# Performance work log

Hardware: AMD Instinct MI355X
Metric: run time of the kernel (lower is better)

## Reference

```python
import jax, jax.numpy as jnp
import numpy as np

N = 10000   # nodes
E = 160000  # edges per layer (avg degree 16)
B = 8       # batch of time windows
CIN = 32
S = 32      # spatial_channels
COUT = 32
NEG_SLOPE = 0.01  # F.leaky_relu default


def _xavier(k, shape):
    bound = np.sqrt(6.0 / (shape[0] + shape[1])).astype(np.float32)
    return jax.random.uniform(k, shape, jnp.float32, -bound, bound)


def setup_inputs() -> dict:
    key = jax.random.key(0)
    ks = jax.random.split(key, 20)
    return {
        "X": jax.random.normal(ks[0], (B, N, CIN), jnp.float32),
        "edge_index0": jax.random.randint(ks[1], (2, E), 0, N, jnp.int32),
        "edge_index1": jax.random.randint(ks[2], (2, E), 0, N, jnp.int32),
        "edge_weight0": jax.random.uniform(ks[3], (E,), jnp.float32),
        "edge_weight1": jax.random.uniform(ks[4], (E,), jnp.float32),
        "res_n_id0": jnp.arange(N, dtype=jnp.int32),
        "res_n_id1": jnp.arange(N, dtype=jnp.int32),
        # layer 1 params
        "Wn1": _xavier(ks[5], (CIN, S)),
        "We1": _xavier(ks[6], (1, S)),
        "Q1": _xavier(ks[7], (S, S)),
        "K1": _xavier(ks[8], (S, S)),
        "att_w1": _xavier(ks[9], (3 * S, 1)),
        "att_b1": jnp.zeros((1,), jnp.float32),
        "out_w1": _xavier(ks[10], (2 * S, S)),
        "out_b1": jnp.zeros((S,), jnp.float32),
        # layer 2 params
        "Wn2": _xavier(ks[11], (S, COUT)),
        "We2": _xavier(ks[12], (1, COUT)),
        "Q2": _xavier(ks[13], (COUT, COUT)),
        "K2": _xavier(ks[14], (COUT, COUT)),
        "att_w2": _xavier(ks[15], (3 * COUT, 1)),
        "att_b2": jnp.zeros((1,), jnp.float32),
        "out_w2": _xavier(ks[16], (2 * COUT, COUT)),
        "out_b2": jnp.zeros((COUT,), jnp.float32),
    }


def _egnn_conv(x_src, x_dst, edge_index, edge_w, Wn, We, Q, K, att_w, att_b, out_w, out_b):
    # x_src: [Ns, B, Cin], x_dst: [Nd, B, Cin], edge_index: [2, E], edge_w: [E]
    xs = x_src @ Wn                              # [Ns, B, O]
    xd = x_dst @ Wn                              # [Nd, B, O]
    ee = edge_w[:, None] @ We                    # [E, O]  (edge_channels = 1)
    src, dst = edge_index[0], edge_index[1]
    xj = xs[src]                                 # [E, B, O] gather source feats
    xi = xd[dst]                                 # [E, B, O] gather target feats
    q = xj @ Q                                   # [E, B, O]
    k = xi @ K                                   # [E, B, O]
    eb = jnp.broadcast_to(ee[:, None, :], q.shape)  # [E, B, O]
    att_feature = jnp.concatenate([q, k, eb], axis=-1)          # [E, B, 3O]
    att = jax.nn.sigmoid(att_feature @ att_w + att_b)           # [E, B, 1]
    msg = att * xj * jax.nn.sigmoid(eb)                         # [E, B, O]
    aggr = jnp.zeros_like(xd).at[dst].add(msg)                  # scatter-add -> [Nd, B, O]
    upd = jnp.concatenate([xd, aggr], axis=-1) @ out_w + out_b  # [Nd, B, O]
    return xd + upd


def reference(X, edge_index0, edge_index1, edge_weight0, edge_weight1,
              res_n_id0, res_n_id1,
              Wn1, We1, Q1, K1, att_w1, att_b1, out_w1, out_b1,
              Wn2, We2, Q2, K2, att_w2, att_b2, out_w2, out_b2):
    h = jnp.transpose(X, (1, 0, 2))              # [N, B, CIN]
    h = _egnn_conv(h, h[res_n_id0], edge_index0, edge_weight0,
                   Wn1, We1, Q1, K1, att_w1, att_b1, out_w1, out_b1)
    h = jax.nn.leaky_relu(h, NEG_SLOPE)
    h = _egnn_conv(h, h[res_n_id1], edge_index1, edge_weight1,
                   Wn2, We2, Q2, K2, att_w2, att_b2, out_w2, out_b2)
    h = jax.nn.leaky_relu(h, NEG_SLOPE)
    return jnp.transpose(h, (1, 0, 2))           # [B, N, COUT]
```

## Files before the change

kernel.cpp:

```cpp
#include <hip/hip_runtime.h>

#define NNODES 10000
#define NEDGES 160000
#define NB 8
#define NC 32
#define CAP 96
#define LUTB 2048
#define EBLKS 625
#define LUTBLKS 128
constexpr float NEG_SLOPE = 0.01f;

__device__ __forceinline__ float sigmoidf_(float x) {
    return 1.0f / (1.0f + __expf(-x));
}

__device__ __forceinline__ unsigned pk2bf(float a, float b) {
    unsigned ua = __float_as_uint(a);
    ua = (ua + 0x7fffu + ((ua >> 16) & 1u)) >> 16;
    unsigned ub = __float_as_uint(b);
    ub = (ub + 0x7fffu + ((ub >> 16) & 1u)) & 0xffff0000u;
    return ua | ub;
}

__global__ __launch_bounds__(256) void prologue_kernel(
    const float* Q1, const float* K1, const float* aw1, const float* We1,
    const float* Q2, const float* K2, const float* aw2, const float* We2,
    const int* __restrict__ ei0, const int* __restrict__ ei1,
    const float* __restrict__ ew0, const float* __restrict__ ew1,
    float* consts, uint2* __restrict__ lut,
    int2* __restrict__ pkw1, int2* __restrict__ pkw2,
    int* __restrict__ cnt,
    unsigned* __restrict__ xs1h, unsigned* __restrict__ xs2h,
    float* __restrict__ sq1, float* __restrict__ sk1,
    const float* __restrict__ X, const float* __restrict__ Wn)
{
    int bx = blockIdx.x;
    int t = threadIdx.x;

    if (bx < 2 * EBLKS) {
        int layer = bx / EBLKS;
        int e = (bx % EBLKS) * 256 + t;
        if (e < NEDGES) {
            const int*   ei = layer ? ei1 : ei0;
            const float* ew = layer ? ew1 : ew0;
            int src = ei[e];
            int dst = ei[NEDGES + e];
            float w = ew[e];
            int pos = atomicAdd(&cnt[layer * NNODES + dst], 1);
            if (pos < CAP) {
                int ix = (int)(w * (float)LUTB);
                ix = min(max(ix, 0), LUTB - 1);
                (layer ? pkw2 : pkw1)[(size_t)dst * CAP + pos] =
                    make_int2(src | (ix << 14), __float_as_int(w));
            }
        }
        return;
    }
    if (bx < 2 * EBLKS + LUTBLKS) {
        int i = (bx - 2 * EBLKS) * 256 + t;
        int layer = i >> 14;
        int bin   = (i >> 3) & (LUTB - 1);
        int o4    = i & 7;
        float w   = (bin + 0.5f) * (1.0f / LUTB);
        const float* We = layer ? We2 : We1;
        float s0 = sigmoidf_(w * We[o4 * 4 + 0]);
        float s1 = sigmoidf_(w * We[o4 * 4 + 1]);
        float s2 = sigmoidf_(w * We[o4 * 4 + 2]);
        float s3 = sigmoidf_(w * We[o4 * 4 + 3]);
        lut[i] = make_uint2(pk2bf(s0, s1), pk2bf(s2, s3));
        if (i < 128) {
            xs1h[(size_t)NNODES * 128 + i] = 0u;
            xs2h[(size_t)NNODES * 128 + i] = 0u;
        }
        return;
    }
    if (bx == 2 * EBLKS + LUTBLKS) {
        if (t < 32) {
            float aq2 = 0.f, ak2 = 0.f;
            for (int s = 0; s < 32; ++s) {
                aq2 += Q2[t * 32 + s] * aw2[s];
                ak2 += K2[t * 32 + s] * aw2[32 + s];
            }
            consts[64 + t] = aq2;
            consts[96 + t] = ak2;
            if (t == 0) {
                float ce1 = 0.f, ce2 = 0.f;
                for (int s = 0; s < 32; ++s) {
                    ce1 += We1[s] * aw1[64 + s];
                    ce2 += We2[s] * aw2[64 + s];
                }
                consts[128] = ce1;
                consts[129] = ce2;
            }
        }
        return;
    }

    __shared__ float wnL[NC * NC];
    __shared__ float aqL[NC], akL[NC];
    __shared__ float xrow[4][NB][NC + 4];
    int w = t >> 6, l = t & 63, b = l >> 3, o4 = l & 7;
    int n = (bx - (2 * EBLKS + LUTBLKS + 1)) * 4 + w;
    for (int i = t; i < NC * NC; i += 256) wnL[i] = Wn[i];
    if (t < 64) {
        int which = t >> 5, o = t & 31;
        const float* M  = which ? K1 : Q1;
        const float* av = aw1 + which * 32;
        float s = 0.f;
        for (int k = 0; k < 32; ++k) s += M[o * 32 + k] * av[k];
        (which ? akL : aqL)[o] = s;
    }
    const float4* X4 = (const float4*)X;
    float4 xv = X4[((size_t)b * NNODES + n) * 8 + o4];
    ((float4*)&xrow[w][b][0])[o4] = xv;
    __syncthreads();
    float4 aq = ((const float4*)aqL)[o4];
    float4 ak = ((const float4*)akL)[o4];
    const float4* wnL4 = (const float4*)wnL;
    float4 acc = {0.f, 0.f, 0.f, 0.f};
    #pragma unroll
    for (int c = 0; c < NC; ++c) {
        float xc = xrow[w][b][c];
        float4 w4 = wnL4[c * 8 + o4];
        acc.x += xc * w4.x; acc.y += xc * w4.y;
        acc.z += xc * w4.z; acc.w += xc * w4.w;
    }
    ((uint2*)xs1h)[(size_t)n * 64 + l] = make_uint2(pk2bf(acc.x, acc.y), pk2bf(acc.z, acc.w));
    float vq = acc.x * aq.x + acc.y * aq.y + acc.z * aq.z + acc.w * aq.w;
    float vk = acc.x * ak.x + acc.y * ak.y + acc.z * ak.z + acc.w * ak.w;
    #pragma unroll
    for (int m = 4; m >= 1; m >>= 1) {
        vq += __shfl_xor(vq, m);
        vk += __shfl_xor(vk, m);
    }
    if (o4 == 0) {
        sq1[n * NB + b] = vq;
        sk1[n * NB + b] = vk;
    }
}

template <int MODE>
__global__ __launch_bounds__(256) void gather_kernel(
    const int* __restrict__ cnt, const int2* __restrict__ pkw,
    const unsigned* __restrict__ xsh,
    const float* __restrict__ sq, const float* __restrict__ sk,
    const uint2* __restrict__ luth,
    const float* __restrict__ abp, const float* __restrict__ consts, int ceoff,
    const float* __restrict__ ow, const float* __restrict__ ob,
    const float* __restrict__ Wn2,
    unsigned* __restrict__ xs2h, float* __restrict__ sq2, float* __restrict__ sk2,
    float* __restrict__ outp)
{
    __shared__ __align__(16) float owL[2 * NC * NC];
    __shared__ __align__(16) float wnL[(MODE == 0) ? NC * NC : 4];

    int t = threadIdx.x, w = t >> 6, l = t & 63, b = l >> 3, o4 = l & 7;
    int n = blockIdx.x * 4 + w;
    for (int i = t; i < 2 * NC * NC; i += 256) owL[i] = ow[i];
    if (MODE == 0)
        for (int i = t; i < NC * NC; i += 256) wnL[i] = Wn2[i];
    __syncthreads();

    const float4* owL4 = (const float4*)owL;
    const float4* wnL4 = (const float4*)wnL;
    const uint2*  XH   = (const uint2*)xsh;
    float ab = abp[0];
    float ce = consts[ceoff];

    int deg = min(cnt[n], CAP - 24);
    const int2* pp = pkw + (size_t)n * CAP;
    float skb = sk[n * NB + b];

    float4 acc = {0.f, 0.f, 0.f, 0.f};
    int2 mc = pp[o4];
    float sqc = sq[(mc.x & 16383) * NB + b];
    for (int c0 = 0; c0 < deg; c0 += 8) {
        int2 mn = pp[c0 + 8 + o4];
        float sqn = sq[(mn.x & 16383) * NB + b];
        float wv = __int_as_float(mc.y);
        float att_own = (c0 + o4 < deg)
                      ? sigmoidf_(sqc + skb + wv * ce + ab) : 0.f;
        #pragma unroll
        for (int j = 0; j < 8; ++j) {
            int spk = __builtin_amdgcn_readlane(mc.x, j);
            int ssrc, six;
            if (c0 + j < deg) {
                ssrc = spk & 16383;
                six  = (spk >> 14) & 2047;
            } else {
                ssrc = NNODES;
                six  = 0;
            }
            uint2 hx = XH[(size_t)ssrc * 64 + l];
            uint2 hg = luth[six * 8 + o4];
            float at = __shfl(att_own, b * 8 + j);
            acc.x += at * __uint_as_float(hg.x << 16)          * __uint_as_float(hx.x << 16);
            acc.y += at * __uint_as_float(hg.x & 0xffff0000u)  * __uint_as_float(hx.x & 0xffff0000u);
            acc.z += at * __uint_as_float(hg.y << 16)          * __uint_as_float(hx.y << 16);
            acc.w += at * __uint_as_float(hg.y & 0xffff0000u)  * __uint_as_float(hx.y & 0xffff0000u);
        }
        mc = mn; sqc = sqn;
    }

    uint2 hv = XH[(size_t)n * 64 + l];
    float4 xv;
    xv.x = __uint_as_float(hv.x << 16);
    xv.y = __uint_as_float(hv.x & 0xffff0000u);
    xv.z = __uint_as_float(hv.y << 16);
    xv.w = __uint_as_float(hv.y & 0xffff0000u);
    float4 u = ((const float4*)ob)[o4];
    #pragma unroll
    for (int cg = 0; cg < 8; ++cg) {
        int sl = b * 8 + cg;
        float xc0 = __shfl(xv.x, sl), xc1 = __shfl(xv.y, sl);
        float xc2 = __shfl(xv.z, sl), xc3 = __shfl(xv.w, sl);
        float ac0 = __shfl(acc.x, sl), ac1 = __shfl(acc.y, sl);
        float ac2 = __shfl(acc.z, sl), ac3 = __shfl(acc.w, sl);
        float4 w10 = owL4[(cg * 4 + 0) * 8 + o4];
        float4 w11 = owL4[(cg * 4 + 1) * 8 + o4];
        float4 w12 = owL4[(cg * 4 + 2) * 8 + o4];
        float4 w13 = owL4[(cg * 4 + 3) * 8 + o4];
        float4 w20 = owL4[(32 + cg * 4 + 0) * 8 + o4];
        float4 w21 = owL4[(32 + cg * 4 + 1) * 8 + o4];
        float4 w22 = owL4[(32 + cg * 4 + 2) * 8 + o4];
        float4 w23 = owL4[(32 + cg * 4 + 3) * 8 + o4];
        u.x += xc0*w10.x + xc1*w11.x + xc2*w12.x + xc3*w13.x
             + ac0*w20.x + ac1*w21.x + ac2*w22.x + ac3*w23.x;
        u.y += xc0*w10.y + xc1*w11.y + xc2*w12.y + xc3*w13.y
             + ac0*w20.y + ac1*w21.y + ac2*w22.y + ac3*w23.y;
        u.z += xc0*w10.z + xc1*w11.z + xc2*w12.z + xc3*w13.z
             + ac0*w20.z + ac1*w21.z + ac2*w22.z + ac3*w23.z;
        u.w += xc0*w10.w + xc1*w11.w + xc2*w12.w + xc3*w13.w
             + ac0*w20.w + ac1*w21.w + ac2*w22.w + ac3*w23.w;
    }
    float4 r;
    r.x = xv.x + u.x; r.y = xv.y + u.y; r.z = xv.z + u.z; r.w = xv.w + u.w;
    r.x = (r.x > 0.f) ? r.x : NEG_SLOPE * r.x;
    r.y = (r.y > 0.f) ? r.y : NEG_SLOPE * r.y;
    r.z = (r.z > 0.f) ? r.z : NEG_SLOPE * r.z;
    r.w = (r.w > 0.f) ? r.w : NEG_SLOPE * r.w;

    if (MODE == 1) {
        ((float4*)outp)[((size_t)b * NNODES + n) * 8 + o4] = r;
    } else {
        float4 a2 = {0.f, 0.f, 0.f, 0.f};
        #pragma unroll
        for (int cg = 0; cg < 8; ++cg) {
            int sl = b * 8 + cg;
            float h0 = __shfl(r.x, sl), h1 = __shfl(r.y, sl);
            float h2 = __shfl(r.z, sl), h3 = __shfl(r.w, sl);
            float4 w0 = wnL4[(cg * 4 + 0) * 8 + o4];
            float4 w1 = wnL4[(cg * 4 + 1) * 8 + o4];
            float4 w2 = wnL4[(cg * 4 + 2) * 8 + o4];
            float4 w3 = wnL4[(cg * 4 + 3) * 8 + o4];
            a2.x += h0*w0.x + h1*w1.x + h2*w2.x + h3*w3.x;
            a2.y += h0*w0.y + h1*w1.y + h2*w2.y + h3*w3.y;
            a2.z += h0*w0.z + h1*w1.z + h2*w2.z + h3*w3.z;
            a2.w += h0*w0.w + h1*w1.w + h2*w2.w + h3*w3.w;
        }
        ((uint2*)xs2h)[(size_t)n * 64 + l] = make_uint2(pk2bf(a2.x, a2.y), pk2bf(a2.z, a2.w));
        float4 aqv = ((const float4*)(consts + 64))[o4];
        float4 akv = ((const float4*)(consts + 96))[o4];
        float vq = a2.x*aqv.x + a2.y*aqv.y + a2.z*aqv.z + a2.w*aqv.w;
        float vk = a2.x*akv.x + a2.y*akv.y + a2.z*akv.z + a2.w*akv.w;
        #pragma unroll
        for (int m = 4; m >= 1; m >>= 1) {
            vq += __shfl_xor(vq, m);
            vk += __shfl_xor(vk, m);
        }
        if (o4 == 0) {
            sq2[n * NB + b] = vq;
            sk2[n * NB + b] = vk;
        }
    }
}

extern "C" void kernel_launch(void* const* d_in, const int* in_sizes, int n_in,
                              void* d_out, int out_size, void* d_ws, size_t ws_size,
                              hipStream_t stream) {
    const float* X    = (const float*)d_in[0];
    const int*   ei0  = (const int*)  d_in[1];
    const int*   ei1  = (const int*)  d_in[2];
    const float* ew0  = (const float*)d_in[3];
    const float* ew1  = (const float*)d_in[4];
    const float* Wn1  = (const float*)d_in[7];
    const float* We1  = (const float*)d_in[8];
    const float* Q1   = (const float*)d_in[9];
    const float* K1   = (const float*)d_in[10];
    const float* aw1  = (const float*)d_in[11];
    const float* ab1  = (const float*)d_in[12];
    const float* ow1  = (const float*)d_in[13];
    const float* ob1  = (const float*)d_in[14];
    const float* Wn2  = (const float*)d_in[15];
    const float* We2  = (const float*)d_in[16];
    const float* Q2   = (const float*)d_in[17];
    const float* K2   = (const float*)d_in[18];
    const float* aw2  = (const float*)d_in[19];
    const float* ab2  = (const float*)d_in[20];
    const float* ow2  = (const float*)d_in[21];
    const float* ob2  = (const float*)d_in[22];

    const size_t ROWH = (size_t)(NNODES + 1) * 128;
    const size_t SS   = (size_t)(NNODES + 1) * NB;
    unsigned* XS1H  = (unsigned*)d_ws;
    unsigned* XS2H  = XS1H + ROWH;
    float* SQ1    = (float*)(XS2H + ROWH);
    float* SK1    = SQ1 + SS;
    float* SQ2    = SK1 + SS;
    float* SK2    = SQ2 + SS;
    float* CONSTS = SK2 + SS;
    uint2* LUTH   = (uint2*)(CONSTS + 160);
    int*   CNT    = (int*)(LUTH + 2 * LUTB * 8);
    int2*  PKW1   = (int2*)(CNT + 2 * NNODES);
    int2*  PKW2   = PKW1 + (size_t)NNODES * CAP;

    hipMemsetAsync(CNT, 0, 2 * NNODES * sizeof(int), stream);
    prologue_kernel<<<2 * EBLKS + LUTBLKS + 1 + NNODES / 4, 256, 0, stream>>>(
        Q1, K1, aw1, We1, Q2, K2, aw2, We2, ei0, ei1, ew0, ew1,
        CONSTS, LUTH, PKW1, PKW2, CNT, XS1H, XS2H, SQ1, SK1, X, Wn1);

    gather_kernel<0><<<NNODES / 4, 256, 0, stream>>>(
        CNT, PKW1, XS1H, SQ1, SK1, LUTH, ab1, CONSTS, 128,
        ow1, ob1, Wn2, XS2H, SQ2, SK2, nullptr);
    gather_kernel<1><<<NNODES / 4, 256, 0, stream>>>(
        CNT + NNODES, PKW2, XS2H, SQ2, SK2, LUTH + LUTB * 8, ab2, CONSTS, 129,
        ow2, ob2, nullptr, nullptr, nullptr, nullptr, (float*)d_out);
}
```

Measured before the change: 101.7 us.

## Precompute per-edge attention bias in prologue and use LDS for output matvecs

The edge-bucketing blocks now compute the edge-weight attention term (w*ce+ab) once per edge and store it in place of the raw weight, so the gather loop skips a multiply-add and two scalar loads. The per-node output and Wn2 matvecs now stage x, aggregate and hidden vectors in shared memory and read them as broadcasts, replacing the many cross-lane shuffles. This adds an LDS round-trip and a block sync in the edge blocks. The e<NEDGES guard was removed, which is safe only because 625*256 equals the edge count exactly.

```diff
diff --git a/kernel.cpp b/kernel.cpp
--- a/kernel.cpp
+++ b/kernel.cpp
@@ -27,6 +27,7 @@
     const float* Q2, const float* K2, const float* aw2, const float* We2,
     const int* __restrict__ ei0, const int* __restrict__ ei1,
     const float* __restrict__ ew0, const float* __restrict__ ew1,
+    const float* __restrict__ ab1, const float* __restrict__ ab2,
     float* consts, uint2* __restrict__ lut,
     int2* __restrict__ pkw1, int2* __restrict__ pkw2,
     int* __restrict__ cnt,
@@ -38,21 +39,29 @@
     int t = threadIdx.x;
 
     if (bx < 2 * EBLKS) {
+        __shared__ float sCE, sAB;
         int layer = bx / EBLKS;
         int e = (bx % EBLKS) * 256 + t;
-        if (e < NEDGES) {
-            const int*   ei = layer ? ei1 : ei0;
-            const float* ew = layer ? ew1 : ew0;
-            int src = ei[e];
-            int dst = ei[NEDGES + e];
-            float w = ew[e];
-            int pos = atomicAdd(&cnt[layer * NNODES + dst], 1);
-            if (pos < CAP) {
-                int ix = (int)(w * (float)LUTB);
-                ix = min(max(ix, 0), LUTB - 1);
-                (layer ? pkw2 : pkw1)[(size_t)dst * CAP + pos] =
-                    make_int2(src | (ix << 14), __float_as_int(w));
-            }
+        const int*   ei = layer ? ei1 : ei0;
+        const float* ew = layer ? ew1 : ew0;
+        int src = ei[e];
+        int dst = ei[NEDGES + e];
+        float w = ew[e];
+        if (t < 32) {
+            const float* We = layer ? We2 : We1;
+            const float* aw = layer ? aw2 : aw1;
+            float p = We[t] * aw[64 + t];
+            #pragma unroll
+            for (int m = 16; m >= 1; m >>= 1) p += __shfl_xor(p, m, 32);
+            if (t == 0) { sCE = p; sAB = (layer ? ab2 : ab1)[0]; }
+        }
+        __syncthreads();
+        int pos = atomicAdd(&cnt[layer * NNODES + dst], 1);
+        if (pos < CAP) {
+            int ix = (int)(w * (float)LUTB);
+            ix = min(max(ix, 0), LUTB - 1);
+            (layer ? pkw2 : pkw1)[(size_t)dst * CAP + pos] =
+                make_int2(src | (ix << 14), __float_as_int(w * sCE + sAB));
         }
         return;
     }
@@ -83,15 +92,6 @@
             }
             consts[64 + t] = aq2;
             consts[96 + t] = ak2;
-            if (t == 0) {
-                float ce1 = 0.f, ce2 = 0.f;
-                for (int s = 0; s < 32; ++s) {
-                    ce1 += We1[s] * aw1[64 + s];
-                    ce2 += We2[s] * aw2[64 + s];
-                }
-                consts[128] = ce1;
-                consts[129] = ce2;
-            }
         }
         return;
     }
@@ -145,7 +145,7 @@
     const unsigned* __restrict__ xsh,
     const float* __restrict__ sq, const float* __restrict__ sk,
     const uint2* __restrict__ luth,
-    const float* __restrict__ abp, const float* __restrict__ consts, int ceoff,
+    const float* __restrict__ consts,
     const float* __restrict__ ow, const float* __restrict__ ob,
     const float* __restrict__ Wn2,
     unsigned* __restrict__ xs2h, float* __restrict__ sq2, float* __restrict__ sk2,
@@ -153,6 +153,8 @@
 {
     __shared__ __align__(16) float owL[2 * NC * NC];
     __shared__ __align__(16) float wnL[(MODE == 0) ? NC * NC : 4];
+    __shared__ __align__(16) float xL[4][NB][NC];
+    __shared__ __align__(16) float aL[4][NB][NC];
 
     int t = threadIdx.x, w = t >> 6, l = t & 63, b = l >> 3, o4 = l & 7;
     int n = blockIdx.x * 4 + w;
@@ -164,8 +166,6 @@
     const float4* owL4 = (const float4*)owL;
     const float4* wnL4 = (const float4*)wnL;
     const uint2*  XH   = (const uint2*)xsh;
-    float ab = abp[0];
-    float ce = consts[ceoff];
 
     int deg = min(cnt[n], CAP - 24);
     const int2* pp = pkw + (size_t)n * CAP;
@@ -177,9 +177,8 @@
     for (int c0 = 0; c0 < deg; c0 += 8) {
         int2 mn = pp[c0 + 8 + o4];
         float sqn = sq[(mn.x & 16383) * NB + b];
-        float wv = __int_as_float(mc.y);
         float att_own = (c0 + o4 < deg)
-                      ? sigmoidf_(sqc + skb + wv * ce + ab) : 0.f;
+                      ? sigmoidf_(sqc + skb + __int_as_float(mc.y)) : 0.f;
         #pragma unroll
         for (int j = 0; j < 8; ++j) {
             int spk = __builtin_amdgcn_readlane(mc.x, j);
@@ -208,30 +207,19 @@
     xv.y = __uint_as_float(hv.x & 0xffff0000u);
     xv.z = __uint_as_float(hv.y << 16);
     xv.w = __uint_as_float(hv.y & 0xffff0000u);
+    ((float4*)&xL[w][b][0])[o4] = xv;
+    ((float4*)&aL[w][b][0])[o4] = acc;
     float4 u = ((const float4*)ob)[o4];
-    #pragma unroll
-    for (int cg = 0; cg < 8; ++cg) {
-        int sl = b * 8 + cg;
-        float xc0 = __shfl(xv.x, sl), xc1 = __shfl(xv.y, sl);
-        float xc2 = __shfl(xv.z, sl), xc3 = __shfl(xv.w, sl);
-        float ac0 = __shfl(acc.x, sl), ac1 = __shfl(acc.y, sl);
-        float ac2 = __shfl(acc.z, sl), ac3 = __shfl(acc.w, sl);
-        float4 w10 = owL4[(cg * 4 + 0) * 8 + o4];
-        float4 w11 = owL4[(cg * 4 + 1) * 8 + o4];
-        float4 w12 = owL4[(cg * 4 + 2) * 8 + o4];
-        float4 w13 = owL4[(cg * 4 + 3) * 8 + o4];
-        float4 w20 = owL4[(32 + cg * 4 + 0) * 8 + o4];
-        float4 w21 = owL4[(32 + cg * 4 + 1) * 8 + o4];
-        float4 w22 = owL4[(32 + cg * 4 + 2) * 8 + o4];
-        float4 w23 = owL4[(32 + cg * 4 + 3) * 8 + o4];
-        u.x += xc0*w10.x + xc1*w11.x + xc2*w12.x + xc3*w13.x
-             + ac0*w20.x + ac1*w21.x + ac2*w22.x + ac3*w23.x;
-        u.y += xc0*w10.y + xc1*w11.y + xc2*w12.y + xc3*w13.y
-             + ac0*w20.y + ac1*w21.y + ac2*w22.y + ac3*w23.y;
-        u.z += xc0*w10.z + xc1*w11.z + xc2*w12.z + xc3*w13.z
-             + ac0*w20.z + ac1*w21.z + ac2*w22.z + ac3*w23.z;
-        u.w += xc0*w10.w + xc1*w11.w + xc2*w12.w + xc3*w13.w
-             + ac0*w20.w + ac1*w21.w + ac2*w22.w + ac3*w23.w;
+    #pragma unroll 4
+    for (int c = 0; c < NC; ++c) {
+        float xc = xL[w][b][c];
+        float ac = aL[w][b][c];
+        float4 w1 = owL4[c * 8 + o4];
+        float4 w2 = owL4[(NC + c) * 8 + o4];
+        u.x += xc * w1.x + ac * w2.x;
+        u.y += xc * w1.y + ac * w2.y;
+        u.z += xc * w1.z + ac * w2.z;
+        u.w += xc * w1.w + ac * w2.w;
     }
     float4 r;
     r.x = xv.x + u.x; r.y = xv.y + u.y; r.z = xv.z + u.z; r.w = xv.w + u.w;
@@ -243,20 +231,16 @@
     if (MODE == 1) {
         ((float4*)outp)[((size_t)b * NNODES + n) * 8 + o4] = r;
     } else {
+        ((float4*)&xL[w][b][0])[o4] = r;
         float4 a2 = {0.f, 0.f, 0.f, 0.f};
-        #pragma unroll
-        for (int cg = 0; cg < 8; ++cg) {
-            int sl = b * 8 + cg;
-            float h0 = __shfl(r.x, sl), h1 = __shfl(r.y, sl);
-            float h2 = __shfl(r.z, sl), h3 = __shfl(r.w, sl);
-            float4 w0 = wnL4[(cg * 4 + 0) * 8 + o4];
-            float4 w1 = wnL4[(cg * 4 + 1) * 8 + o4];
-            float4 w2 = wnL4[(cg * 4 + 2) * 8 + o4];
-            float4 w3 = wnL4[(cg * 4 + 3) * 8 + o4];
-            a2.x += h0*w0.x + h1*w1.x + h2*w2.x + h3*w3.x;
-            a2.y += h0*w0.y + h1*w1.y + h2*w2.y + h3*w3.y;
-            a2.z += h0*w0.z + h1*w1.z + h2*w2.z + h3*w3.z;
-            a2.w += h0*w0.w + h1*w1.w + h2*w2.w + h3*w3.w;
+        #pragma unroll 4
+        for (int c = 0; c < NC; ++c) {
+            float hc = xL[w][b][c];
+            float4 w0 = wnL4[c * 8 + o4];
+            a2.x += hc * w0.x;
+            a2.y += hc * w0.y;
+            a2.z += hc * w0.z;
+            a2.w += hc * w0.w;
         }
         ((uint2*)xs2h)[(size_t)n * 64 + l] = make_uint2(pk2bf(a2.x, a2.y), pk2bf(a2.z, a2.w));
         float4 aqv = ((const float4*)(consts + 64))[o4];
@@ -316,13 +300,13 @@
 
     hipMemsetAsync(CNT, 0, 2 * NNODES * sizeof(int), stream);
     prologue_kernel<<<2 * EBLKS + LUTBLKS + 1 + NNODES / 4, 256, 0, stream>>>(
-        Q1, K1, aw1, We1, Q2, K2, aw2, We2, ei0, ei1, ew0, ew1,
+        Q1, K1, aw1, We1, Q2, K2, aw2, We2, ei0, ei1, ew0, ew1, ab1, ab2,
         CONSTS, LUTH, PKW1, PKW2, CNT, XS1H, XS2H, SQ1, SK1, X, Wn1);
 
     gather_kernel<0><<<NNODES / 4, 256, 0, stream>>>(
-        CNT, PKW1, XS1H, SQ1, SK1, LUTH, ab1, CONSTS, 128,
+        CNT, PKW1, XS1H, SQ1, SK1, LUTH, CONSTS,
         ow1, ob1, Wn2, XS2H, SQ2, SK2, nullptr);
     gather_kernel<1><<<NNODES / 4, 256, 0, stream>>>(
-        CNT + NNODES, PKW2, XS2H, SQ2, SK2, LUTH + LUTB * 8, ab2, CONSTS, 129,
+        CNT + NNODES, PKW2, XS2H, SQ2, SK2, LUTH + LUTB * 8, CONSTS,
         ow2, ob2, nullptr, nullptr, nullptr, nullptr, (float*)d_out);
 }
```

Result: faster. 92.81 us (-8.7%).
